# Performance work log

Measured on AMD Instinct MI355X. Metric: run time of the kernel, lower is better.

The kernel has to match this reference:

```python
import jax, jax.numpy as jnp
import numpy as np

EMBED_DIM = 1024
HIDDEN_DIM = 4096
NUM_EXPERTS = 8
TOP_K = 2


def setup_inputs() -> dict:
    key = jax.random.key(0)
    ks = jax.random.split(key, 5)
    x = jax.random.normal(ks[0], (2, 2048, EMBED_DIM), dtype=jnp.float32)
    Wg = jax.random.normal(ks[1], (EMBED_DIM, NUM_EXPERTS), dtype=jnp.float32) * 0.02
    W1 = jax.random.normal(ks[2], (NUM_EXPERTS, EMBED_DIM, HIDDEN_DIM), dtype=jnp.float32) * 0.02
    W3 = jax.random.normal(ks[3], (NUM_EXPERTS, EMBED_DIM, HIDDEN_DIM), dtype=jnp.float32) * 0.02
    W2 = jax.random.normal(ks[4], (NUM_EXPERTS, HIDDEN_DIM, EMBED_DIM), dtype=jnp.float32) * 0.02
    return {"x": x, "Wg": Wg, "W1": W1, "W3": W3, "W2": W2}


def reference(x, Wg, W1, W3, W2):
    # Gate: linear projection to num_experts logits
    gate = jnp.einsum("bsd,de->bse", x, Wg)  # [B,S,E]
    top_vals, top_idx = jax.lax.top_k(gate, TOP_K)  # [B,S,K]
    sel_w = jax.nn.softmax(top_vals, axis=-1)  # softmax over top-k values
    # Scatter selected weights into dense [B,S,E] (zeros for unselected experts)
    dense_w = jnp.sum(
        jax.nn.one_hot(top_idx, NUM_EXPERTS, dtype=sel_w.dtype) * sel_w[..., None],
        axis=-2,
    )  # [B,S,E]
    # Per-expert SwiGLU FFN; weight=0 for tokens not routed to expert e,
    # so the weighted-sum form is mathematically identical to masked dispatch.
    out = jnp.zeros_like(x)
    for e in range(NUM_EXPERTS):
        h = jax.nn.swish(jnp.einsum("bsd,dh->bsh", x, W1[e])) * jnp.einsum(
            "bsd,dh->bsh", x, W3[e]
        )
        out = out + dense_w[..., e:e + 1] * jnp.einsum("bsh,hd->bsd", h, W2[e])
    return out
```

## Files before the change

### kernel.cpp

```cpp
#include <hip/hip_runtime.h>
#include <hip/hip_bf16.h>
#include <stdint.h>

#define D_EMBED 1024
#define D_HID   4096
#define N_TOK   4096
#define N_EXP   8
#define CAP     4096
#define NROWA   8448

typedef __attribute__((ext_vector_type(4))) float f32x4;
typedef __attribute__((ext_vector_type(8))) short bf16x8;

__device__ __forceinline__ unsigned short f2bf(float f) {
    unsigned int u = __builtin_bit_cast(unsigned int, f);
    u += 0x7fffu + ((u >> 16) & 1u);
    return (unsigned short)(u >> 16);
}
__device__ __forceinline__ float bf2f(unsigned short h) {
    unsigned int u = ((unsigned int)h) << 16;
    return __builtin_bit_cast(float, u);
}
__device__ __forceinline__ void gload_lds16(const void* g, void* l) {
    __builtin_amdgcn_global_load_lds(
        (const __attribute__((address_space(1))) unsigned int*)g,
        (__attribute__((address_space(3))) unsigned int*)l, 16, 0, 0);
}

__global__ __launch_bounds__(256) void pack_all(const float* __restrict__ W1,
                                                const float* __restrict__ W3,
                                                const float* __restrict__ W2,
                                                unsigned short* __restrict__ wt13,
                                                unsigned short* __restrict__ wt2) {
    int b = blockIdx.x;
    if (b < 32768) {
        int idx = b * 256 + threadIdx.x;
        int pc = idx & 8191, s = (idx >> 13) & 127, e = idx >> 20;
        int g = pc >> 4;
        int rc = ((g >> 1) << 4) + (pc & 15);
        const float* src = (g & 1 ? W3 : W1) + (size_t)e * (D_EMBED * D_HID)
                         + (size_t)(s * 8) * D_HID + rc;
        bf16x8 o;
#pragma unroll
        for (int j = 0; j < 8; ++j) o[j] = (short)f2bf(src[(size_t)j * D_HID]);
        *reinterpret_cast<bf16x8*>(wt13 + (size_t)e * (D_EMBED * 2 * D_HID)
                                   + ((size_t)s * (2 * D_HID) + pc) * 8) = o;
    } else {
        int idx = (b - 32768) * 256 + threadIdx.x;
        int col = idx & 1023, s = (idx >> 10) & 511, e = idx >> 19;
        const float* src = W2 + (size_t)e * (D_HID * D_EMBED) + (size_t)(s * 8) * D_EMBED + col;
        bf16x8 o;
#pragma unroll
        for (int j = 0; j < 8; ++j) o[j] = (short)f2bf(src[(size_t)j * D_EMBED]);
        *reinterpret_cast<bf16x8*>(wt2 + (size_t)e * (D_HID * D_EMBED)
                                   + ((size_t)s * D_EMBED + col) * 8) = o;
    }
}

__global__ __launch_bounds__(256) void gate_kernel(const float* __restrict__ x,
                                                   const float* __restrict__ Wg,
                                                   int* __restrict__ counts,
                                                   int* __restrict__ toks,
                                                   float* __restrict__ wgts,
                                                   int* __restrict__ slots) {
    int wave = threadIdx.x >> 6;
    int lane = threadIdx.x & 63;
    int tok = blockIdx.x * 4 + wave;
    const float* xp = x + (size_t)tok * D_EMBED;
    float acc[8] = {0, 0, 0, 0, 0, 0, 0, 0};
#pragma unroll
    for (int i = 0; i < 16; ++i) {
        int d = lane + 64 * i;
        float xv = xp[d];
        f32x4 w0 = *reinterpret_cast<const f32x4*>(Wg + (size_t)d * 8);
        f32x4 w1 = *reinterpret_cast<const f32x4*>(Wg + (size_t)d * 8 + 4);
        acc[0] += xv * w0[0]; acc[1] += xv * w0[1]; acc[2] += xv * w0[2]; acc[3] += xv * w0[3];
        acc[4] += xv * w1[0]; acc[5] += xv * w1[1]; acc[6] += xv * w1[2]; acc[7] += xv * w1[3];
    }
#pragma unroll
    for (int e = 0; e < 8; ++e)
        for (int s = 32; s; s >>= 1) acc[e] += __shfl_xor(acc[e], s, 64);
    if (lane == 0) {
        int i0 = 0; float v0 = acc[0];
#pragma unroll
        for (int e = 1; e < 8; ++e) if (acc[e] > v0) { v0 = acc[e]; i0 = e; }
        int i1 = -1; float v1 = -1e30f;
#pragma unroll
        for (int e = 0; e < 8; ++e) if (e != i0 && acc[e] > v1) { v1 = acc[e]; i1 = e; }
        float ex = __expf(v1 - v0);
        float w0 = 1.0f / (1.0f + ex);
        float w1 = 1.0f - w0;
        int p0 = atomicAdd(&counts[i0], 1);
        toks[i0 * CAP + p0] = tok; wgts[i0 * CAP + p0] = w0; slots[i0 * CAP + p0] = 0;
        int p1 = atomicAdd(&counts[i1], 1);
        toks[i1 * CAP + p1] = tok; wgts[i1 * CAP + p1] = w1; slots[i1 * CAP + p1] = 1;
    }
}

__global__ __launch_bounds__(256) void gather_x_kernel(
    const float* __restrict__ x, const int* __restrict__ counts,
    const int* __restrict__ toks, const int* __restrict__ slots,
    int* __restrict__ tok2row, unsigned short* __restrict__ xg) {
    int rt = blockIdx.x;
    int e = -1, tb = 0, osum = 0, rowbase = 0, cnt = 0, off = 0;
    for (int ee = 0; ee < N_EXP; ++ee) {
        int c = counts[ee];
        int nt = (c + 63) >> 6;
        if (rt < tb + nt) { e = ee; rowbase = (rt - tb) << 6; cnt = c; off = osum; break; }
        tb += nt; osum += c;
    }
    if (e < 0) return;
    int kb = blockIdx.y;
    int t = threadIdx.x;
    if (kb == 0 && t < 64) {
        int pos = rowbase + t;
        if (pos < cnt) {
            int i = e * CAP + pos;
            tok2row[toks[i] * 2 + slots[i]] = off + pos;
        }
    }
    __shared__ unsigned short lds[64][72];
    int r = t >> 2, ck = t & 3;
    int pos = rowbase + r;
    unsigned short tmp[16];
    if (pos < cnt) {
        int tok = toks[e * CAP + pos];
        const float* src = x + (size_t)tok * D_EMBED + kb * 64 + ck * 16;
#pragma unroll
        for (int i = 0; i < 4; ++i) {
            f32x4 v = *reinterpret_cast<const f32x4*>(src + i * 4);
#pragma unroll
            for (int j = 0; j < 4; ++j) tmp[i * 4 + j] = f2bf(v[j]);
        }
    } else {
#pragma unroll
        for (int i = 0; i < 16; ++i) tmp[i] = 0;
    }
#pragma unroll
    for (int i = 0; i < 16; ++i) lds[r][ck * 16 + i] = tmp[i];
    __syncthreads();
    int sl = t >> 5, rr = (t & 31) * 2;
#pragma unroll
    for (int w = 0; w < 2; ++w) {
        int rw = rr + w;
        if (rowbase + rw >= cnt) continue;
        bf16x8 o;
#pragma unroll
        for (int j = 0; j < 8; ++j) o[j] = (short)lds[rw][sl * 8 + j];
        *reinterpret_cast<bf16x8*>(xg + ((size_t)(kb * 8 + sl) * NROWA + off + rowbase + rw) * 8) = o;
    }
}

__global__ __launch_bounds__(512, 4) void gemm1_kernel(
    const unsigned short* __restrict__ xg,
    const unsigned short* __restrict__ wt13,
    const int* __restrict__ counts,
    const float* __restrict__ wgts,
    unsigned short* __restrict__ hp) {
    int rt = blockIdx.y;
    int e = -1, tb = 0, osum = 0, rowbase = 0, cnt = 0, off = 0;
#pragma unroll 1
    for (int ee = 0; ee < N_EXP; ++ee) {
        int c = counts[ee];
        int nt = (c + 127) >> 7;
        if (rt < tb + nt) { e = ee; rowbase = (rt - tb) << 7; cnt = c; off = osum; break; }
        tb += nt; osum += c;
    }
    if (e < 0) return;

    __shared__ __align__(16) char lds[2][24576];

    int t = threadIdx.x, lane = t & 63, w = t >> 6;
    int wr = w >> 2, wc = w & 3;
    int q = lane >> 4, p = lane & 15;

    const size_t ASTEP = (size_t)4 * NROWA * 16;
    const size_t BSTEP = (size_t)4 * (2 * D_HID) * 16;
    const char* aS = (const char*)xg + ((size_t)(t >> 7) * NROWA + off + rowbase + (t & 127)) * 16;
    const char* bS0 = (const char*)wt13 + (size_t)e * D_EMBED * 2 * D_HID * 2
                    + ((size_t)(t >> 8) * (2 * D_HID) + blockIdx.x * 256 + (t & 255)) * 16;
    const char* bS1 = bS0 + (size_t)2 * (2 * D_HID) * 16;

    int wslot = 0;
    auto STG = [&]() {
        char* L = &lds[wslot][0];
        wslot ^= 1;
        gload_lds16(aS, L + t * 16);                 aS += ASTEP;
        gload_lds16(bS0, L + 8192 + t * 16);         bS0 += BSTEP;
        gload_lds16(bS1, L + 16384 + t * 16);        bS1 += BSTEP;
    };

    f32x4 acc[4][4] = {};

    STG();
#pragma unroll 1
    for (int h = 0; h < 32; ++h) {
        if (h < 31) STG();
        if (h < 31) asm volatile("s_waitcnt vmcnt(3)" ::: "memory");
        else        asm volatile("s_waitcnt vmcnt(0)" ::: "memory");
        __builtin_amdgcn_s_barrier();
        __builtin_amdgcn_sched_barrier(0);
        const char* L = &lds[h & 1][0];
        bf16x8 af[4], bf[4];
#pragma unroll
        for (int m = 0; m < 4; ++m)
            af[m] = *reinterpret_cast<const bf16x8*>(L + (q * 128 + wr * 64 + m * 16 + p) * 16);
#pragma unroll
        for (int n = 0; n < 4; ++n)
            bf[n] = *reinterpret_cast<const bf16x8*>(L + 8192 + (q * 256 + wc * 64 + n * 16 + p) * 16);
        __builtin_amdgcn_s_setprio(1);
#pragma unroll
        for (int n = 0; n < 4; ++n)
#pragma unroll
            for (int m = 0; m < 4; ++m)
                acc[m][n] = __builtin_amdgcn_mfma_f32_16x16x32_bf16(af[m], bf[n], acc[m][n], 0, 0, 0);
        __builtin_amdgcn_s_setprio(0);
    }

#pragma unroll
    for (int m = 0; m < 4; ++m) {
#pragma unroll
        for (int reg = 0; reg < 4; ++reg) {
            int rl = wr * 64 + m * 16 + q * 4 + reg;
            int grow = rowbase + rl;
            if (grow >= cnt) continue;
            float wgt = wgts[e * CAP + grow];
            size_t row = (size_t)(off + grow);
#pragma unroll
            for (int np = 0; np < 2; ++np) {
                float a1 = acc[m][2 * np][reg];
                float a3 = acc[m][2 * np + 1][reg];
                float hv = (a1 / (1.0f + __expf(-a1))) * a3 * wgt;
                int rc = (blockIdx.x * 8 + wc * 2 + np) * 16 + p;
                hp[((size_t)(rc >> 3) * NROWA + row) * 8 + (rc & 7)] = f2bf(hv);
            }
        }
    }
}

__global__ __launch_bounds__(512, 4) void gemm2_kernel(
    const unsigned short* __restrict__ hp,
    const unsigned short* __restrict__ wt2,
    const int* __restrict__ counts,
    unsigned short* __restrict__ pbuf) {
    int rt = blockIdx.y;
    int e = -1, tb = 0, osum = 0, rowbase = 0, cnt = 0, off = 0;
#pragma unroll 1
    for (int ee = 0; ee < N_EXP; ++ee) {
        int c = counts[ee];
        int nt = (c + 127) >> 7;
        if (rt < tb + nt) { e = ee; rowbase = (rt - tb) << 7; cnt = c; off = osum; break; }
        tb += nt; osum += c;
    }
    if (e < 0) return;
    int s2 = blockIdx.z;

    __shared__ __align__(16) char lds[2][24576];

    int t = threadIdx.x, lane = t & 63, w = t >> 6;
    int wr = w >> 2, wc = w & 3;
    int q = lane >> 4, p = lane & 15;

    const size_t ASTEP = (size_t)4 * NROWA * 16;
    const size_t BSTEP = (size_t)4 * D_EMBED * 16;
    const char* aS = (const char*)hp
        + ((size_t)(s2 * 256 + (t >> 7)) * NROWA + off + rowbase + (t & 127)) * 16;
    const char* bS0 = (const char*)wt2 + (size_t)e * D_HID * D_EMBED * 2
        + ((size_t)(s2 * 256 + (t >> 8)) * D_EMBED + blockIdx.x * 256 + (t & 255)) * 16;
    const char* bS1 = bS0 + (size_t)2 * D_EMBED * 16;

    int wslot = 0;
    auto STG = [&]() {
        char* L = &lds[wslot][0];
        wslot ^= 1;
        gload_lds16(aS, L + t * 16);                 aS += ASTEP;
        gload_lds16(bS0, L + 8192 + t * 16);         bS0 += BSTEP;
        gload_lds16(bS1, L + 16384 + t * 16);        bS1 += BSTEP;
    };

    f32x4 acc[4][4] = {};

    STG();
#pragma unroll 1
    for (int h = 0; h < 64; ++h) {
        if (h < 63) STG();
        if (h < 63) asm volatile("s_waitcnt vmcnt(3)" ::: "memory");
        else        asm volatile("s_waitcnt vmcnt(0)" ::: "memory");
        __builtin_amdgcn_s_barrier();
        __builtin_amdgcn_sched_barrier(0);
        const char* L = &lds[h & 1][0];
        bf16x8 af[4], bf[4];
#pragma unroll
        for (int m = 0; m < 4; ++m)
            af[m] = *reinterpret_cast<const bf16x8*>(L + (q * 128 + wr * 64 + m * 16 + p) * 16);
#pragma unroll
        for (int n = 0; n < 4; ++n)
            bf[n] = *reinterpret_cast<const bf16x8*>(L + 8192 + (q * 256 + wc * 64 + n * 16 + p) * 16);
        __builtin_amdgcn_s_setprio(1);
#pragma unroll
        for (int n = 0; n < 4; ++n)
#pragma unroll
            for (int m = 0; m < 4; ++m)
                acc[m][n] = __builtin_amdgcn_mfma_f32_16x16x32_bf16(af[m], bf[n], acc[m][n], 0, 0, 0);
        __builtin_amdgcn_s_setprio(0);
    }

    unsigned short* pb = pbuf + (size_t)s2 * 8192 * D_EMBED;
#pragma unroll
    for (int m = 0; m < 4; ++m)
#pragma unroll
        for (int reg = 0; reg < 4; ++reg) {
            int rl = wr * 64 + m * 16 + q * 4 + reg;
            int grow = rowbase + rl;
            if (grow >= cnt) continue;
            unsigned short* dst = pb + (size_t)(off + grow) * D_EMBED + blockIdx.x * 256 + wc * 64;
#pragma unroll
            for (int n = 0; n < 4; ++n) dst[n * 16 + p] = f2bf(acc[m][n][reg]);
        }
}

__global__ __launch_bounds__(256) void combine_kernel(const unsigned short* __restrict__ pbuf,
                                                      const int* __restrict__ tok2row,
                                                      float* __restrict__ out) {
    int i = blockIdx.x * 256 + threadIdx.x;
    int tok = i >> 7, c0 = (i & 127) * 8;
    int r0 = tok2row[tok * 2], r1 = tok2row[tok * 2 + 1];
    const size_t SP = (size_t)8192 * D_EMBED;
    float s[8] = {0, 0, 0, 0, 0, 0, 0, 0};
#pragma unroll
    for (int sp = 0; sp < 2; ++sp) {
        bf16x8 a = *reinterpret_cast<const bf16x8*>(pbuf + sp * SP + (size_t)r0 * D_EMBED + c0);
        bf16x8 b = *reinterpret_cast<const bf16x8*>(pbuf + sp * SP + (size_t)r1 * D_EMBED + c0);
#pragma unroll
        for (int j = 0; j < 8; ++j)
            s[j] += bf2f((unsigned short)a[j]) + bf2f((unsigned short)b[j]);
    }
    float* op = out + (size_t)tok * D_EMBED + c0;
    f32x4 lo = {s[0], s[1], s[2], s[3]}, hi = {s[4], s[5], s[6], s[7]};
    *reinterpret_cast<f32x4*>(op) = lo;
    *reinterpret_cast<f32x4*>(op + 4) = hi;
}

extern "C" void kernel_launch(void* const* d_in, const int* in_sizes, int n_in,
                              void* d_out, int out_size, void* d_ws, size_t ws_size,
                              hipStream_t stream) {
    const float* x  = (const float*)d_in[0];
    const float* Wg = (const float*)d_in[1];
    const float* W1 = (const float*)d_in[2];
    const float* W3 = (const float*)d_in[3];
    const float* W2 = (const float*)d_in[4];
    float* out = (float*)d_out;

    char* ws = (char*)d_ws;
    size_t szW = (size_t)N_EXP * D_EMBED * D_HID;
    unsigned short* wt13 = (unsigned short*)ws; ws += szW * 2 * 2;
    unsigned short* wt2  = (unsigned short*)ws; ws += szW * 2;
    unsigned short* hp   = (unsigned short*)ws; ws += (size_t)(D_HID / 8) * NROWA * 8 * 2;
    unsigned short* xg   = (unsigned short*)ws; ws += (size_t)(D_EMBED / 8) * NROWA * 8 * 2;
    int*   toks    = (int*)ws;   ws += (size_t)N_EXP * CAP * 4;
    float* wgts    = (float*)ws; ws += (size_t)N_EXP * CAP * 4;
    int*   slots   = (int*)ws;   ws += (size_t)N_EXP * CAP * 4;
    int*   tok2row = (int*)ws;   ws += (size_t)N_TOK * 2 * 4;
    int*   counts  = (int*)ws;   ws += 8 * 4;
    unsigned short* pbuf = (unsigned short*)wt13;

    hipMemsetAsync(counts, 0, 8 * sizeof(int), stream);

    pack_all<<<49152, 256, 0, stream>>>(W1, W3, W2, wt13, wt2);
    gate_kernel<<<N_TOK / 4, 256, 0, stream>>>(x, Wg, counts, toks, wgts, slots);
    gather_x_kernel<<<dim3(136, D_EMBED / 64), 256, 0, stream>>>(x, counts, toks, slots, tok2row, xg);
    gemm1_kernel<<<dim3(32, 72), 512, 0, stream>>>(xg, wt13, counts, wgts, hp);
    gemm2_kernel<<<dim3(4, 72, 2), 512, 0, stream>>>(hp, wt2, counts, pbuf);
    combine_kernel<<<(N_TOK * 128) / 256, 256, 0, stream>>>(pbuf, tok2row, out);
}
```

Measured before the change: 487.4 us.

## Fuse gate into pack kernel and shrink GEMM tiles to 128x128 with 4-way split-K

Merges the gating kernel into the weight-pack launch as extra blocks, removing one launch. Both expert GEMMs move from 512-thread 128x256 tiles to 256-thread 128x128 tiles with smaller LDS buffers, doubling the grid. gemm2 now uses a 4-way K split, so the combine kernel reads four partial buffers. The aim is more blocks and better occupancy, paid for with more weight re-reads, more partial-sum traffic, and a larger pbuf footprint aliased onto wt13.

```diff
diff --git a/kernel.cpp b/kernel.cpp
--- a/kernel.cpp
+++ b/kernel.cpp
@@ -27,11 +27,17 @@
         (__attribute__((address_space(3))) unsigned int*)l, 16, 0, 0);
 }
 
-__global__ __launch_bounds__(256) void pack_all(const float* __restrict__ W1,
-                                                const float* __restrict__ W3,
-                                                const float* __restrict__ W2,
-                                                unsigned short* __restrict__ wt13,
-                                                unsigned short* __restrict__ wt2) {
+__global__ __launch_bounds__(256) void pack_gate(const float* __restrict__ W1,
+                                                 const float* __restrict__ W3,
+                                                 const float* __restrict__ W2,
+                                                 const float* __restrict__ x,
+                                                 const float* __restrict__ Wg,
+                                                 unsigned short* __restrict__ wt13,
+                                                 unsigned short* __restrict__ wt2,
+                                                 int* __restrict__ counts,
+                                                 int* __restrict__ toks,
+                                                 float* __restrict__ wgts,
+                                                 int* __restrict__ slots) {
     int b = blockIdx.x;
     if (b < 32768) {
         int idx = b * 256 + threadIdx.x;
@@ -45,7 +51,7 @@
         for (int j = 0; j < 8; ++j) o[j] = (short)f2bf(src[(size_t)j * D_HID]);
         *reinterpret_cast<bf16x8*>(wt13 + (size_t)e * (D_EMBED * 2 * D_HID)
                                    + ((size_t)s * (2 * D_HID) + pc) * 8) = o;
-    } else {
+    } else if (b < 49152) {
         int idx = (b - 32768) * 256 + threadIdx.x;
         int col = idx & 1023, s = (idx >> 10) & 511, e = idx >> 19;
         const float* src = W2 + (size_t)e * (D_HID * D_EMBED) + (size_t)(s * 8) * D_EMBED + col;
@@ -54,46 +60,40 @@
         for (int j = 0; j < 8; ++j) o[j] = (short)f2bf(src[(size_t)j * D_EMBED]);
         *reinterpret_cast<bf16x8*>(wt2 + (size_t)e * (D_HID * D_EMBED)
                                    + ((size_t)s * D_EMBED + col) * 8) = o;
-    }
-}
-
-__global__ __launch_bounds__(256) void gate_kernel(const float* __restrict__ x,
-                                                   const float* __restrict__ Wg,
-                                                   int* __restrict__ counts,
-                                                   int* __restrict__ toks,
-                                                   float* __restrict__ wgts,
-                                                   int* __restrict__ slots) {
-    int wave = threadIdx.x >> 6;
-    int lane = threadIdx.x & 63;
-    int tok = blockIdx.x * 4 + wave;
-    const float* xp = x + (size_t)tok * D_EMBED;
-    float acc[8] = {0, 0, 0, 0, 0, 0, 0, 0};
-#pragma unroll
-    for (int i = 0; i < 16; ++i) {
-        int d = lane + 64 * i;
-        float xv = xp[d];
-        f32x4 w0 = *reinterpret_cast<const f32x4*>(Wg + (size_t)d * 8);
-        f32x4 w1 = *reinterpret_cast<const f32x4*>(Wg + (size_t)d * 8 + 4);
-        acc[0] += xv * w0[0]; acc[1] += xv * w0[1]; acc[2] += xv * w0[2]; acc[3] += xv * w0[3];
-        acc[4] += xv * w1[0]; acc[5] += xv * w1[1]; acc[6] += xv * w1[2]; acc[7] += xv * w1[3];
-    }
-#pragma unroll
-    for (int e = 0; e < 8; ++e)
-        for (int s = 32; s; s >>= 1) acc[e] += __shfl_xor(acc[e], s, 64);
-    if (lane == 0) {
-        int i0 = 0; float v0 = acc[0];
-#pragma unroll
-        for (int e = 1; e < 8; ++e) if (acc[e] > v0) { v0 = acc[e]; i0 = e; }
-        int i1 = -1; float v1 = -1e30f;
-#pragma unroll
-        for (int e = 0; e < 8; ++e) if (e != i0 && acc[e] > v1) { v1 = acc[e]; i1 = e; }
-        float ex = __expf(v1 - v0);
-        float w0 = 1.0f / (1.0f + ex);
-        float w1 = 1.0f - w0;
-        int p0 = atomicAdd(&counts[i0], 1);
-        toks[i0 * CAP + p0] = tok; wgts[i0 * CAP + p0] = w0; slots[i0 * CAP + p0] = 0;
-        int p1 = atomicAdd(&counts[i1], 1);
-        toks[i1 * CAP + p1] = tok; wgts[i1 * CAP + p1] = w1; slots[i1 * CAP + p1] = 1;
+    } else {
+        int gb = b - 49152;
+        int wave = threadIdx.x >> 6;
+        int lane = threadIdx.x & 63;
+        int tok = gb * 4 + wave;
+        const float* xp = x + (size_t)tok * D_EMBED;
+        float acc[8] = {0, 0, 0, 0, 0, 0, 0, 0};
+#pragma unroll
+        for (int i = 0; i < 16; ++i) {
+            int d = lane + 64 * i;
+            float xv = xp[d];
+            f32x4 w0 = *reinterpret_cast<const f32x4*>(Wg + (size_t)d * 8);
+            f32x4 w1 = *reinterpret_cast<const f32x4*>(Wg + (size_t)d * 8 + 4);
+            acc[0] += xv * w0[0]; acc[1] += xv * w0[1]; acc[2] += xv * w0[2]; acc[3] += xv * w0[3];
+            acc[4] += xv * w1[0]; acc[5] += xv * w1[1]; acc[6] += xv * w1[2]; acc[7] += xv * w1[3];
+        }
+#pragma unroll
+        for (int e = 0; e < 8; ++e)
+            for (int s = 32; s; s >>= 1) acc[e] += __shfl_xor(acc[e], s, 64);
+        if (lane == 0) {
+            int i0 = 0; float v0 = acc[0];
+#pragma unroll
+            for (int e = 1; e < 8; ++e) if (acc[e] > v0) { v0 = acc[e]; i0 = e; }
+            int i1 = -1; float v1 = -1e30f;
+#pragma unroll
+            for (int e = 0; e < 8; ++e) if (e != i0 && acc[e] > v1) { v1 = acc[e]; i1 = e; }
+            float ex = __expf(v1 - v0);
+            float w0 = 1.0f / (1.0f + ex);
+            float w1 = 1.0f - w0;
+            int p0 = atomicAdd(&counts[i0], 1);
+            toks[i0 * CAP + p0] = tok; wgts[i0 * CAP + p0] = w0; slots[i0 * CAP + p0] = 0;
+            int p1 = atomicAdd(&counts[i1], 1);
+            toks[i1 * CAP + p1] = tok; wgts[i1 * CAP + p1] = w1; slots[i1 * CAP + p1] = 1;
+        }
     }
 }
 
@@ -151,7 +151,7 @@
     }
 }
 
-__global__ __launch_bounds__(512, 4) void gemm1_kernel(
+__global__ __launch_bounds__(256, 4) void gemm1_kernel(
     const unsigned short* __restrict__ xg,
     const unsigned short* __restrict__ wt13,
     const int* __restrict__ counts,
@@ -168,26 +168,29 @@
     }
     if (e < 0) return;
 
-    __shared__ __align__(16) char lds[2][24576];
+    __shared__ __align__(16) char lds[2][16384];
 
     int t = threadIdx.x, lane = t & 63, w = t >> 6;
-    int wr = w >> 2, wc = w & 3;
+    int wr = w >> 1, wc = w & 1;
     int q = lane >> 4, p = lane & 15;
 
     const size_t ASTEP = (size_t)4 * NROWA * 16;
     const size_t BSTEP = (size_t)4 * (2 * D_HID) * 16;
+    const size_t A2 = (size_t)2 * NROWA * 16;
+    const size_t B2 = (size_t)2 * (2 * D_HID) * 16;
     const char* aS = (const char*)xg + ((size_t)(t >> 7) * NROWA + off + rowbase + (t & 127)) * 16;
-    const char* bS0 = (const char*)wt13 + (size_t)e * D_EMBED * 2 * D_HID * 2
-                    + ((size_t)(t >> 8) * (2 * D_HID) + blockIdx.x * 256 + (t & 255)) * 16;
-    const char* bS1 = bS0 + (size_t)2 * (2 * D_HID) * 16;
+    const char* bS = (const char*)wt13 + (size_t)e * D_EMBED * 2 * D_HID * 2
+                   + ((size_t)(t >> 7) * (2 * D_HID) + blockIdx.x * 128 + (t & 127)) * 16;
 
     int wslot = 0;
     auto STG = [&]() {
         char* L = &lds[wslot][0];
         wslot ^= 1;
-        gload_lds16(aS, L + t * 16);                 aS += ASTEP;
-        gload_lds16(bS0, L + 8192 + t * 16);         bS0 += BSTEP;
-        gload_lds16(bS1, L + 16384 + t * 16);        bS1 += BSTEP;
+        gload_lds16(aS, L + t * 16);
+        gload_lds16(aS + A2, L + 4096 + t * 16);
+        gload_lds16(bS, L + 8192 + t * 16);
+        gload_lds16(bS + B2, L + 12288 + t * 16);
+        aS += ASTEP; bS += BSTEP;
     };
 
     f32x4 acc[4][4] = {};
@@ -196,7 +199,7 @@
 #pragma unroll 1
     for (int h = 0; h < 32; ++h) {
         if (h < 31) STG();
-        if (h < 31) asm volatile("s_waitcnt vmcnt(3)" ::: "memory");
+        if (h < 31) asm volatile("s_waitcnt vmcnt(4)" ::: "memory");
         else        asm volatile("s_waitcnt vmcnt(0)" ::: "memory");
         __builtin_amdgcn_s_barrier();
         __builtin_amdgcn_sched_barrier(0);
@@ -207,7 +210,7 @@
             af[m] = *reinterpret_cast<const bf16x8*>(L + (q * 128 + wr * 64 + m * 16 + p) * 16);
 #pragma unroll
         for (int n = 0; n < 4; ++n)
-            bf[n] = *reinterpret_cast<const bf16x8*>(L + 8192 + (q * 256 + wc * 64 + n * 16 + p) * 16);
+            bf[n] = *reinterpret_cast<const bf16x8*>(L + 8192 + (q * 128 + wc * 64 + n * 16 + p) * 16);
         __builtin_amdgcn_s_setprio(1);
 #pragma unroll
         for (int n = 0; n < 4; ++n)
@@ -231,14 +234,14 @@
                 float a1 = acc[m][2 * np][reg];
                 float a3 = acc[m][2 * np + 1][reg];
                 float hv = (a1 / (1.0f + __expf(-a1))) * a3 * wgt;
-                int rc = (blockIdx.x * 8 + wc * 2 + np) * 16 + p;
+                int rc = (blockIdx.x * 4 + wc * 2 + np) * 16 + p;
                 hp[((size_t)(rc >> 3) * NROWA + row) * 8 + (rc & 7)] = f2bf(hv);
             }
         }
     }
 }
 
-__global__ __launch_bounds__(512, 4) void gemm2_kernel(
+__global__ __launch_bounds__(256, 4) void gemm2_kernel(
     const unsigned short* __restrict__ hp,
     const unsigned short* __restrict__ wt2,
     const int* __restrict__ counts,
@@ -255,36 +258,39 @@
     if (e < 0) return;
     int s2 = blockIdx.z;
 
-    __shared__ __align__(16) char lds[2][24576];
+    __shared__ __align__(16) char lds[2][16384];
 
     int t = threadIdx.x, lane = t & 63, w = t >> 6;
-    int wr = w >> 2, wc = w & 3;
+    int wr = w >> 1, wc = w & 1;
     int q = lane >> 4, p = lane & 15;
 
     const size_t ASTEP = (size_t)4 * NROWA * 16;
     const size_t BSTEP = (size_t)4 * D_EMBED * 16;
+    const size_t A2 = (size_t)2 * NROWA * 16;
+    const size_t B2 = (size_t)2 * D_EMBED * 16;
     const char* aS = (const char*)hp
-        + ((size_t)(s2 * 256 + (t >> 7)) * NROWA + off + rowbase + (t & 127)) * 16;
-    const char* bS0 = (const char*)wt2 + (size_t)e * D_HID * D_EMBED * 2
-        + ((size_t)(s2 * 256 + (t >> 8)) * D_EMBED + blockIdx.x * 256 + (t & 255)) * 16;
-    const char* bS1 = bS0 + (size_t)2 * D_EMBED * 16;
+        + ((size_t)(s2 * 128 + (t >> 7)) * NROWA + off + rowbase + (t & 127)) * 16;
+    const char* bS = (const char*)wt2 + (size_t)e * D_HID * D_EMBED * 2
+        + ((size_t)(s2 * 128 + (t >> 7)) * D_EMBED + blockIdx.x * 128 + (t & 127)) * 16;
 
     int wslot = 0;
     auto STG = [&]() {
         char* L = &lds[wslot][0];
         wslot ^= 1;
-        gload_lds16(aS, L + t * 16);                 aS += ASTEP;
-        gload_lds16(bS0, L + 8192 + t * 16);         bS0 += BSTEP;
-        gload_lds16(bS1, L + 16384 + t * 16);        bS1 += BSTEP;
+        gload_lds16(aS, L + t * 16);
+        gload_lds16(aS + A2, L + 4096 + t * 16);
+        gload_lds16(bS, L + 8192 + t * 16);
+        gload_lds16(bS + B2, L + 12288 + t * 16);
+        aS += ASTEP; bS += BSTEP;
     };
 
     f32x4 acc[4][4] = {};
 
     STG();
 #pragma unroll 1
-    for (int h = 0; h < 64; ++h) {
-        if (h < 63) STG();
-        if (h < 63) asm volatile("s_waitcnt vmcnt(3)" ::: "memory");
+    for (int h = 0; h < 32; ++h) {
+        if (h < 31) STG();
+        if (h < 31) asm volatile("s_waitcnt vmcnt(4)" ::: "memory");
         else        asm volatile("s_waitcnt vmcnt(0)" ::: "memory");
         __builtin_amdgcn_s_barrier();
         __builtin_amdgcn_sched_barrier(0);
@@ -295,7 +301,7 @@
             af[m] = *reinterpret_cast<const bf16x8*>(L + (q * 128 + wr * 64 + m * 16 + p) * 16);
 #pragma unroll
         for (int n = 0; n < 4; ++n)
-            bf[n] = *reinterpret_cast<const bf16x8*>(L + 8192 + (q * 256 + wc * 64 + n * 16 + p) * 16);
+            bf[n] = *reinterpret_cast<const bf16x8*>(L + 8192 + (q * 128 + wc * 64 + n * 16 + p) * 16);
         __builtin_amdgcn_s_setprio(1);
 #pragma unroll
         for (int n = 0; n < 4; ++n)
@@ -313,7 +319,7 @@
             int rl = wr * 64 + m * 16 + q * 4 + reg;
             int grow = rowbase + rl;
             if (grow >= cnt) continue;
-            unsigned short* dst = pb + (size_t)(off + grow) * D_EMBED + blockIdx.x * 256 + wc * 64;
+            unsigned short* dst = pb + (size_t)(off + grow) * D_EMBED + blockIdx.x * 128 + wc * 64;
 #pragma unroll
             for (int n = 0; n < 4; ++n) dst[n * 16 + p] = f2bf(acc[m][n][reg]);
         }
@@ -328,7 +334,7 @@
     const size_t SP = (size_t)8192 * D_EMBED;
     float s[8] = {0, 0, 0, 0, 0, 0, 0, 0};
 #pragma unroll
-    for (int sp = 0; sp < 2; ++sp) {
+    for (int sp = 0; sp < 4; ++sp) {
         bf16x8 a = *reinterpret_cast<const bf16x8*>(pbuf + sp * SP + (size_t)r0 * D_EMBED + c0);
         bf16x8 b = *reinterpret_cast<const bf16x8*>(pbuf + sp * SP + (size_t)r1 * D_EMBED + c0);
 #pragma unroll
@@ -366,10 +372,10 @@
 
     hipMemsetAsync(counts, 0, 8 * sizeof(int), stream);
 
-    pack_all<<<49152, 256, 0, stream>>>(W1, W3, W2, wt13, wt2);
-    gate_kernel<<<N_TOK / 4, 256, 0, stream>>>(x, Wg, counts, toks, wgts, slots);
+    pack_gate<<<49152 + N_TOK / 4, 256, 0, stream>>>(W1, W3, W2, x, Wg, wt13, wt2,
+                                                     counts, toks, wgts, slots);
     gather_x_kernel<<<dim3(136, D_EMBED / 64), 256, 0, stream>>>(x, counts, toks, slots, tok2row, xg);
-    gemm1_kernel<<<dim3(32, 72), 512, 0, stream>>>(xg, wt13, counts, wgts, hp);
-    gemm2_kernel<<<dim3(4, 72, 2), 512, 0, stream>>>(hp, wt2, counts, pbuf);
+    gemm1_kernel<<<dim3(64, 72), 256, 0, stream>>>(xg, wt13, counts, wgts, hp);
+    gemm2_kernel<<<dim3(8, 72, 4), 256, 0, stream>>>(hp, wt2, counts, pbuf);
     combine_kernel<<<(N_TOK * 128) / 256, 256, 0, stream>>>(pbuf, tok2row, out);
 }
```

New measurement: 472.9 us. 1.03x faster.
